# Kernel tuning notes

Measured on AMD Instinct MI355X. Metric: run time of the kernel, lower is better.

Reference implementation:

```python
import jax, jax.numpy as jnp
import numpy as np

B, N, C, G, K = 4, 6000, 91, 32, 100
IMG = 800.0
SCORE_TH = 0.05
NMS_TH = 0.5
MATCH_TH = 0.5
MIN_SIZE = 0.01
BBOX_CLIP = float(np.log(1000.0 / 16.0))
WX, WY, WW, WH = 10.0, 10.0, 5.0, 5.0


def _make_boxes(key, shape_prefix):
    k1, k2 = jax.random.split(key)
    xy = jax.random.uniform(k1, shape_prefix + (2,), minval=0.0, maxval=IMG - 130.0)
    wh = jax.random.uniform(k2, shape_prefix + (2,), minval=8.0, maxval=128.0)
    return jnp.concatenate([xy, xy + wh], axis=-1)


def setup_inputs() -> dict:
    key = jax.random.key(0)
    k1, k2, k3, k4, k5 = jax.random.split(key, 5)
    return {
        "class_logits": 2.0 * jax.random.normal(k1, (B * N, C), dtype=jnp.float32),
        "box_regression": jax.random.normal(k2, (B * N, C * 4), dtype=jnp.float32),
        "proposals": _make_boxes(k3, (B, N)),
        "gt_boxes": _make_boxes(k4, (B, G)),
        "gt_labels": jax.random.randint(k5, (B, G), 1, C),
    }


def _box_iou(a, b):
    # a [G,4], b [N,4] -> [G,N]
    area_a = (a[:, 2] - a[:, 0]) * (a[:, 3] - a[:, 1])
    area_b = (b[:, 2] - b[:, 0]) * (b[:, 3] - b[:, 1])
    lt = jnp.maximum(a[:, None, :2], b[None, :, :2])
    rb = jnp.minimum(a[:, None, 2:], b[None, :, 2:])
    wh = jnp.clip(rb - lt, 0.0)
    inter = wh[..., 0] * wh[..., 1]
    return inter / (area_a[:, None] + area_b[None, :] - inter)


def _decode(rel, props):
    # torchvision BoxCoder.decode; rel [N,C,4], props [N,4]
    w = props[:, 2] - props[:, 0]
    h = props[:, 3] - props[:, 1]
    cx = props[:, 0] + 0.5 * w
    cy = props[:, 1] + 0.5 * h
    dx = rel[..., 0] / WX
    dy = rel[..., 1] / WY
    dw = jnp.minimum(rel[..., 2] / WW, BBOX_CLIP)
    dh = jnp.minimum(rel[..., 3] / WH, BBOX_CLIP)
    pcx = dx * w[:, None] + cx[:, None]
    pcy = dy * h[:, None] + cy[:, None]
    pw = jnp.exp(dw) * w[:, None]
    ph = jnp.exp(dh) * h[:, None]
    return jnp.stack([pcx - 0.5 * pw, pcy - 0.5 * ph, pcx + 0.5 * pw, pcy + 0.5 * ph], axis=-1)


def _image(logits, reg, props, gtb, gtl):
    # --- assign_targets_to_proposals (Matcher, low=high=0.5, no low-quality matches) ---
    iou = _box_iou(gtb, props)                      # [G, N]
    best = iou.max(axis=0)
    mi = jnp.argmax(iou, axis=0)
    matched = jnp.where(best >= MATCH_TH, mi, -1)   # -1 == BELOW_LOW_THRESHOLD
    assigned = jnp.where(matched >= 0, gtl[jnp.clip(matched, 0)], 0)

    # --- postprocess_detections ---
    scores = jax.nn.softmax(logits, axis=-1)[:, 1:].reshape(-1)                       # [N*(C-1)]
    boxes = jnp.clip(_decode(reg.reshape(N, C, 4), props)[:, 1:], 0.0, IMG)
    boxes = boxes.reshape(-1, 4)                                                      # [N*(C-1),4]
    labels = jnp.tile(jnp.arange(1, C), N)                                            # [N*(C-1)]
    ws = boxes[:, 2] - boxes[:, 0]
    hs = boxes[:, 3] - boxes[:, 1]
    valid = (scores > SCORE_TH) & (ws >= MIN_SIZE) & (hs >= MIN_SIZE)
    s0 = jnp.where(valid, scores, -jnp.inf)
    # batched_nms trick: offset boxes by label so cross-class IoU is 0
    off = boxes + (labels.astype(boxes.dtype) * (IMG + 1.0))[:, None]
    off_area = (off[:, 2] - off[:, 0]) * (off[:, 3] - off[:, 1])

    def step(s, _):
        i = jnp.argmax(s)
        sc = s[i]
        b = off[i]
        lt = jnp.maximum(off[:, :2], b[:2])
        rb = jnp.minimum(off[:, 2:], b[2:])
        wh = jnp.clip(rb - lt, 0.0)
        inter = wh[:, 0] * wh[:, 1]
        iou_all = inter / (off_area + (b[2] - b[0]) * (b[3] - b[1]) - inter)
        s = jnp.where(iou_all > NMS_TH, -jnp.inf, s)  # suppress (includes self)
        ok = jnp.isfinite(sc)
        ob = jnp.where(ok, boxes[i], 0.0)
        osc = jnp.where(ok, sc, 0.0)
        ol = jnp.where(ok, labels[i], -1)
        return s, (ob, osc, ol)

    _, (kb, ksc, kl) = jax.lax.scan(step, s0, None, length=K)
    return kb, ksc, kl, assigned, matched


def reference(class_logits, box_regression, proposals, gt_boxes, gt_labels):
    logits = class_logits.reshape(B, N, C)
    reg = box_regression.reshape(B, N, C * 4)
    kb, ksc, kl, assigned, matched = jax.vmap(_image)(logits, reg, proposals, gt_boxes, gt_labels)
    dets = jnp.concatenate([kb, ksc[..., None]], axis=-1)  # [B, K, 5]
    return dets, kl, assigned, matched
```

## Files before the change

kernel.cpp:

```cpp
#include <hip/hip_runtime.h>
#include <math.h>

#define NB 4
#define NN 6000
#define NC 91
#define NG 32
#define NK 100
#define NCLS (NC - 1)
#define NBUC (NB * NCLS)
#define SLOTS_MAX 2048
#define CUR_STRIDE 32
#define PMAX 512
#define MATW 256
#define MPB 4096
#define RS_BLOCKS 6000

#define SCORE_TH 0.05f
#define NMS_TH 0.5f
#define MATCH_TH 0.5f
#define MIN_SIZE 0.01f
#define BBOX_CLIP 4.135166556742356f
#define C_SUP 0.5000000298023223876953125

#define CFENCE() asm volatile("" ::: "memory")

__device__ __forceinline__ bool decode_one(
    const float* __restrict__ reg, const float* __restrict__ props,
    float l, float m, float s0, int row, int c, float out[5])
{
    float score = __fdiv_rn(expf(__fsub_rn(l, m)), s0);

    const float4 p = *reinterpret_cast<const float4*>(props + (size_t)row * 4);
    float w  = __fsub_rn(p.z, p.x);
    float h  = __fsub_rn(p.w, p.y);
    float cx = __fadd_rn(p.x, __fmul_rn(0.5f, w));
    float cy = __fadd_rn(p.y, __fmul_rn(0.5f, h));

    const float4 r4 = *reinterpret_cast<const float4*>(
        reg + (size_t)row * (NC * 4) + (size_t)c * 4);
    float dx = __fdiv_rn(r4.x, 10.0f);
    float dy = __fdiv_rn(r4.y, 10.0f);
    float dw = fminf(__fdiv_rn(r4.z, 5.0f), BBOX_CLIP);
    float dh = fminf(__fdiv_rn(r4.w, 5.0f), BBOX_CLIP);

    float pcx = __fadd_rn(__fmul_rn(dx, w), cx);
    float pcy = __fadd_rn(__fmul_rn(dy, h), cy);
    float pw  = __fmul_rn(expf(dw), w);
    float ph  = __fmul_rn(expf(dh), h);

    float x1 = __fsub_rn(pcx, __fmul_rn(0.5f, pw));
    float y1 = __fsub_rn(pcy, __fmul_rn(0.5f, ph));
    float x2 = __fadd_rn(pcx, __fmul_rn(0.5f, pw));
    float y2 = __fadd_rn(pcy, __fmul_rn(0.5f, ph));
    x1 = fminf(fmaxf(x1, 0.0f), 800.0f);
    y1 = fminf(fmaxf(y1, 0.0f), 800.0f);
    x2 = fminf(fmaxf(x2, 0.0f), 800.0f);
    y2 = fminf(fmaxf(y2, 0.0f), 800.0f);

    out[0] = score; out[1] = x1; out[2] = y1; out[3] = x2; out[4] = y2;
    float ws_ = __fsub_rn(x2, x1);
    float hs_ = __fsub_rn(y2, y1);
    return (score > SCORE_TH) && (ws_ >= MIN_SIZE) && (hs_ >= MIN_SIZE);
}

__global__ __launch_bounds__(256) void fused_kernel(
    const float* __restrict__ logits, const float* __restrict__ reg,
    const float* __restrict__ props, const float* __restrict__ gtb,
    const int* __restrict__ gtl,
    float* __restrict__ out_assigned, float* __restrict__ out_matched,
    int* __restrict__ cursors, float* __restrict__ ent, int slots)
{
    int bid = blockIdx.x;
    if (bid < RS_BLOCKS) {
        int wid = threadIdx.x >> 6, lane = threadIdx.x & 63;
        int row = bid * 4 + wid;
        const float* rp = logits + (size_t)row * NC;
        float l0 = rp[lane];
        float l1 = (lane < NC - 64) ? rp[64 + lane] : -INFINITY;
        float m = fmaxf(fmaxf(-INFINITY, l0), l1);
        for (int o = 32; o; o >>= 1) m = fmaxf(m, __shfl_down(m, o));
        m = __shfl(m, 0);
        float s = __fadd_rn(__fadd_rn(0.0f, expf(__fsub_rn(l0, m))),
                            expf(__fsub_rn(l1, m)));
        for (int o = 32; o; o >>= 1) s = __fadd_rn(s, __shfl_down(s, o));
        float s0 = __shfl(s, 0);
        float thr = __fadd_rn(m, logf(__fmul_rn(0.04f, s0)));

        int b = row / NN;
        int nprop = row - b * NN;

        if (lane >= 1 && l0 > thr) {
            float o[5];
            if (decode_one(reg, props, l0, m, s0, row, lane, o)) {
                int c = lane;
                int g = b * NCLS + (c - 1);
                int pos = atomicAdd(&cursors[g * CUR_STRIDE], 1);
                if (pos < slots) {
                    float* e = ent + ((size_t)g * slots + pos) * 8;
                    *reinterpret_cast<float4*>(e) =
                        make_float4(o[1], o[2], o[3], o[4]);
                    *reinterpret_cast<float2*>(e + 4) =
                        make_float2(o[0], (float)(nprop * NCLS + (c - 1)));
                }
            }
        }
        if (lane < NC - 64 && l1 > thr) {
            float o[5];
            int c = lane + 64;
            if (decode_one(reg, props, l1, m, s0, row, c, o)) {
                int g = b * NCLS + (c - 1);
                int pos = atomicAdd(&cursors[g * CUR_STRIDE], 1);
                if (pos < slots) {
                    float* e = ent + ((size_t)g * slots + pos) * 8;
                    *reinterpret_cast<float4*>(e) =
                        make_float4(o[1], o[2], o[3], o[4]);
                    *reinterpret_cast<float2*>(e + 4) =
                        make_float2(o[0], (float)(nprop * NCLS + (c - 1)));
                }
            }
        }
    } else {
        int t = (bid - RS_BLOCKS) * 256 + threadIdx.x;
        if (t >= NB * NN) return;
        int b = t / NN;
        const float4 p = *reinterpret_cast<const float4*>(props + (size_t)t * 4);
        float parea = __fmul_rn(__fsub_rn(p.z, p.x), __fsub_rn(p.w, p.y));
        float best = -1.0f; int bi = -1;
        for (int g = 0; g < NG; ++g) {
            const float4 q = *reinterpret_cast<const float4*>(gtb + ((size_t)b * NG + g) * 4);
            float garea = __fmul_rn(__fsub_rn(q.z, q.x), __fsub_rn(q.w, q.y));
            float ltx = fmaxf(q.x, p.x), lty = fmaxf(q.y, p.y);
            float rbx = fminf(q.z, p.z), rby = fminf(q.w, p.w);
            float wx = fmaxf(__fsub_rn(rbx, ltx), 0.0f);
            float wy = fmaxf(__fsub_rn(rby, lty), 0.0f);
            float inter = __fmul_rn(wx, wy);
            float iou = __fdiv_rn(inter, __fsub_rn(__fadd_rn(garea, parea), inter));
            if (iou > best) { best = iou; bi = g; }
        }
        int matched = (best >= MATCH_TH) ? bi : -1;
        int assigned = (matched >= 0) ? gtl[b * NG + matched] : 0;
        out_matched[t]  = (float)matched;
        out_assigned[t] = (float)assigned;
    }
}

__device__ void nms_glb(int g, int n, float* __restrict__ E, float tb, float cls,
                        float* __restrict__ selbuf, int* __restrict__ selcnt)
{
    int lane = threadIdx.x & 63;
    int kout = 0;
    for (int k = 0; k < NK; ++k) {
        float bv = -INFINITY, boi = INFINITY; int bi = -1;
        for (int i = lane; i < n; i += 64) {
            float v = E[(size_t)i * 8 + 4], oi = E[(size_t)i * 8 + 5];
            if (v > bv || (v == bv && oi < boi)) { bv = v; boi = oi; bi = i; }
        }
        int wl = lane;
        for (int o = 1; o < 64; o <<= 1) {
            float v2 = __shfl_xor(bv, o); float o2 = __shfl_xor(boi, o);
            int l2 = __shfl_xor(wl, o);
            bool bt = (v2 > bv) || (v2 == bv && o2 < boi);
            bv = bt ? v2 : bv; boi = bt ? o2 : boi; wl = bt ? l2 : wl;
        }
        if (bv == -INFINITY) break;
        int wi = __shfl(bi, wl);
        float sx1 = E[(size_t)wi * 8 + 0], sy1 = E[(size_t)wi * 8 + 1];
        float sx2 = E[(size_t)wi * 8 + 2], sy2 = E[(size_t)wi * 8 + 3];
        if (lane == wl) {
            float* so = selbuf + ((size_t)g * NK + k) * 8;
            so[0] = bv; so[1] = sx1; so[2] = sy1; so[3] = sx2; so[4] = sy2;
            so[5] = cls; so[6] = boi; so[7] = 0.0f;
        }
        float bx1 = __fadd_rn(sx1, tb), by1 = __fadd_rn(sy1, tb);
        float bx2 = __fadd_rn(sx2, tb), by2 = __fadd_rn(sy2, tb);
        float sar = __fmul_rn(__fsub_rn(bx2, bx1), __fsub_rn(by2, by1));
        for (int i = lane; i < n; i += 64) {
            float v = E[(size_t)i * 8 + 4];
            if (v == -INFINITY) continue;
            float ox1 = __fadd_rn(E[(size_t)i * 8 + 0], tb);
            float oy1 = __fadd_rn(E[(size_t)i * 8 + 1], tb);
            float ox2 = __fadd_rn(E[(size_t)i * 8 + 2], tb);
            float oy2 = __fadd_rn(E[(size_t)i * 8 + 3], tb);
            float oar = __fmul_rn(__fsub_rn(ox2, ox1), __fsub_rn(oy2, oy1));
            float ltx = fmaxf(ox1, bx1), lty = fmaxf(oy1, by1);
            float rbx = fminf(ox2, bx2), rby = fminf(oy2, by2);
            float wx = fmaxf(__fsub_rn(rbx, ltx), 0.0f);
            float wy = fmaxf(__fsub_rn(rby, lty), 0.0f);
            float inter = __fmul_rn(wx, wy);
            float den = __fsub_rn(__fadd_rn(oar, sar), inter);
            if ((double)inter > C_SUP * (double)den) E[(size_t)i * 8 + 4] = -INFINITY;
        }
        kout = k + 1;
    }
    if (lane == 0) selcnt[g] = kout;
}

template <int CAP>
__device__ __forceinline__ float selN(const float a[CAP], int j) {
    float r = a[0];
#pragma unroll
    for (int i = 1; i < CAP; ++i) r = (j == i) ? a[i] : r;
    return r;
}
__device__ __forceinline__ float rdlane(float v, int l) {
    return __uint_as_float(
        (unsigned)__builtin_amdgcn_readlane((int)__float_as_uint(v), l));
}
__device__ __forceinline__ unsigned long long rdlane64(unsigned long long v, int l) {
    unsigned lo = (unsigned)__builtin_amdgcn_readlane((int)(unsigned)v, l);
    unsigned hi = (unsigned)__builtin_amdgcn_readlane((int)(unsigned)(v >> 32), l);
    return ((unsigned long long)hi << 32) | lo;
}

template <int CAP>
__device__ __forceinline__ int sweep_reg(
    int lane, int n, float tb,
    const float* sx1, const float* sy1, const float* sx2, const float* sy2,
    int* acc)
{
    float ox1[CAP], oy1[CAP], ox2[CAP], oy2[CAP], oar[CAP];
    unsigned alive = 0;
#pragma unroll
    for (int j = 0; j < CAP; ++j) {
        int sidx = lane * CAP + j;
        if (sidx < n) {
            float a  = __fadd_rn(sx1[sidx], tb);
            float b_ = __fadd_rn(sy1[sidx], tb);
            float c_ = __fadd_rn(sx2[sidx], tb);
            float d_ = __fadd_rn(sy2[sidx], tb);
            ox1[j] = a; oy1[j] = b_; ox2[j] = c_; oy2[j] = d_;
            oar[j] = __fmul_rn(__fsub_rn(c_, a), __fsub_rn(d_, b_));
            alive |= 1u << j;
        } else {
            ox1[j] = 0.f; oy1[j] = 0.f; ox2[j] = 0.f; oy2[j] = 0.f; oar[j] = 0.f;
        }
    }
    int kout = 0;
    while (kout < NK) {
        unsigned long long bal = __ballot(alive != 0u);
        if (!bal) break;
        int fl = (int)__ffsll(bal) - 1;
        unsigned am = (unsigned)__builtin_amdgcn_readlane((int)alive, fl);
        int js = __ffs(am) - 1;
        float bx1 = rdlane(selN<CAP>(ox1, js), fl);
        float by1 = rdlane(selN<CAP>(oy1, js), fl);
        float bx2 = rdlane(selN<CAP>(ox2, js), fl);
        float by2 = rdlane(selN<CAP>(oy2, js), fl);
        float bar = rdlane(selN<CAP>(oar, js), fl);
        if (lane == 0) acc[kout] = fl * CAP + js;
        kout++;
        unsigned kill = 0;
#pragma unroll
        for (int j = 0; j < CAP; ++j) {
            float ltx = fmaxf(ox1[j], bx1), lty = fmaxf(oy1[j], by1);
            float rbx = fminf(ox2[j], bx2), rby = fminf(oy2[j], by2);
            float wx = fmaxf(__fsub_rn(rbx, ltx), 0.0f);
            float wy = fmaxf(__fsub_rn(rby, lty), 0.0f);
            float inter = __fmul_rn(wx, wy);
            float den = __fsub_rn(__fadd_rn(oar[j], bar), inter);
            if ((double)inter > C_SUP * (double)den) kill |= 1u << j;
        }
        alive &= ~kill;
    }
    return kout;
}

__global__ __launch_bounds__(512) void bucket_nms_kernel(
    const int* __restrict__ cursors, int slots,
    float* __restrict__ entries,
    float* __restrict__ selbuf, int* __restrict__ selcnt)
{
    int g = blockIdx.x;
    int n = cursors[g * CUR_STRIDE]; if (n > slots) n = slots;
    int tid = threadIdx.x;
    if (n == 0) { if (tid == 0) selcnt[g] = 0; return; }
    float* E = entries + (size_t)g * slots * 8;
    float cls = (float)(g % NCLS + 1);
    float tb = __fmul_rn(cls, 801.0f);

    if (n > PMAX) {
        if (tid < 64) nms_glb(g, n, E, tb, cls, selbuf, selcnt);
        return;
    }

    __shared__ unsigned skhi[PMAX], sklo[PMAX];
    __shared__ int sperm[PMAX];
    __shared__ float sx1[PMAX], sy1[PMAX], sx2[PMAX], sy2[PMAX];
    __shared__ unsigned long long dmask[MATW * 4];
    __shared__ int acc[NK];
    __shared__ int s_kout, s_fb;

    int P = 64; while (P < n) P <<= 1;

    for (int i = tid; i < P; i += 512) {
        if (i < n) {
            const float2 kv = *reinterpret_cast<const float2*>(E + (size_t)i * 8 + 4);
            skhi[i] = __float_as_uint(kv.x);
            sklo[i] = ~((unsigned)kv.y);
        } else { skhi[i] = 0u; sklo[i] = 0u; }
        sperm[i] = i;
    }
    __syncthreads();
    for (int k = 2; k <= P; k <<= 1) {
        for (int j = k >> 1; j > 0; j >>= 1) {
            bool cross = (j >= 128);
            if (cross) __syncthreads();
            for (int t = tid; t < (P >> 1); t += 512) {
                int i = ((t & ~(j - 1)) << 1) | (t & (j - 1));
                int l = i | j;
                unsigned ah = skhi[i], al = sklo[i], ch = skhi[l], cl_ = sklo[l];
                bool alt = (ah < ch) || (ah == ch && al < cl_);
                bool agt = (ah > ch) || (ah == ch && al > cl_);
                bool sw = ((i & k) == 0) ? alt : agt;
                if (sw) {
                    skhi[i] = ch; sklo[i] = cl_; skhi[l] = ah; sklo[l] = al;
                    int tp = sperm[i]; sperm[i] = sperm[l]; sperm[l] = tp;
                }
            }
            if (cross) __syncthreads();
            else CFENCE();
        }
    }
    __syncthreads();
    for (int i = tid; i < n; i += 512) {
        const float4 v = *reinterpret_cast<const float4*>(E + (size_t)sperm[i] * 8);
        sx1[i] = v.x; sy1[i] = v.y; sx2[i] = v.z; sy2[i] = v.w;
    }
    __syncthreads();

    int W = (n < MATW) ? n : MATW;
    int nchunk = (W + 63) >> 6;
    int wv = tid >> 6, lane = tid & 63;

    float jx1[4], jy1[4], jx2[4], jy2[4], jar[4];
#pragma unroll
    for (int c = 0; c < 4; ++c) {
        int j = c * 64 + lane;
        if (j < W) {
            float a  = __fadd_rn(sx1[j], tb);
            float b_ = __fadd_rn(sy1[j], tb);
            float c_ = __fadd_rn(sx2[j], tb);
            float d_ = __fadd_rn(sy2[j], tb);
            jx1[c] = a; jy1[c] = b_; jx2[c] = c_; jy2[c] = d_;
            jar[c] = __fmul_rn(__fsub_rn(c_, a), __fsub_rn(d_, b_));
        } else {
            jx1[c] = 0.f; jy1[c] = 0.f; jx2[c] = 0.f; jy2[c] = 0.f; jar[c] = 0.f;
        }
    }
    {
        int i0 = wv;
        float nx1 = 0.f, ny1 = 0.f, nx2 = 0.f, ny2 = 0.f;
        if (i0 < W) { nx1 = sx1[i0]; ny1 = sy1[i0]; nx2 = sx2[i0]; ny2 = sy2[i0]; }
        for (int i = i0; i < W; i += 8) {
            float rx1 = nx1, ry1 = ny1, rx2 = nx2, ry2 = ny2;
            int ni = i + 8;
            if (ni < W) { nx1 = sx1[ni]; ny1 = sy1[ni]; nx2 = sx2[ni]; ny2 = sy2[ni]; }
            float bx1 = __fadd_rn(rx1, tb), by1 = __fadd_rn(ry1, tb);
            float bx2 = __fadd_rn(rx2, tb), by2 = __fadd_rn(ry2, tb);
            float bar = __fmul_rn(__fsub_rn(bx2, bx1), __fsub_rn(by2, by1));
            int ic = i >> 6;
#pragma unroll
            for (int c = 0; c < 4; ++c) {
                if (c >= ic && c < nchunk) {
                    bool jv = (c * 64 + lane) < W;
                    float ltx = fmaxf(jx1[c], bx1), lty = fmaxf(jy1[c], by1);
                    float rbx = fminf(jx2[c], bx2), rby = fminf(jy2[c], by2);
                    float wx = fmaxf(__fsub_rn(rbx, ltx), 0.0f);
                    float wy = fmaxf(__fsub_rn(rby, lty), 0.0f);
                    float inter = __fmul_rn(wx, wy);
                    float den = __fsub_rn(__fadd_rn(jar[c], bar), inter);
                    bool sup = jv && ((double)inter > C_SUP * (double)den);
                    unsigned long long w64 = __ballot(sup);
                    if (lane == 0) dmask[i * 4 + c] = w64;
                }
            }
        }
    }
    __syncthreads();

    if (tid < 64) {
        unsigned long long a0 = 0, a1 = 0, a2 = 0, a3 = 0;
        {
            int rem = W;
            a0 = (rem >= 64) ? ~0ull : ((rem > 0) ? ((1ull << rem) - 1) : 0); rem -= 64;
            a1 = (rem >= 64) ? ~0ull : ((rem > 0) ? ((1ull << rem) - 1) : 0); rem -= 64;
            a2 = (rem >= 64) ? ~0ull : ((rem > 0) ? ((1ull << rem) - 1) : 0); rem -= 64;
            a3 = (rem >= 64) ? ~0ull : ((rem > 0) ? ((1ull << rem) - 1) : 0);
        }
        int kout = 0;
        while (kout < NK) {
            int cand;
            if      (a0) cand = (int)__ffsll(a0) - 1;
            else if (a1) cand = 64  + (int)__ffsll(a1) - 1;
            else if (a2) cand = 128 + (int)__ffsll(a2) - 1;
            else if (a3) cand = 192 + (int)__ffsll(a3) - 1;
            else break;
            if (lane == 0) acc[kout] = cand;
            kout++;
            unsigned long long mrow = (lane < 4) ? dmask[cand * 4 + lane] : 0ull;
            a0 &= ~rdlane64(mrow, 0);
            a1 &= ~rdlane64(mrow, 1);
            a2 &= ~rdlane64(mrow, 2);
            a3 &= ~rdlane64(mrow, 3);
        }
        if (lane == 0) {
            s_kout = kout;
            s_fb = (kout < NK && n > W) ? 1 : 0;
        }
    }
    __syncthreads();

    if (s_fb) {
        if (tid < 64) {
            int kout = sweep_reg<8>(lane, n, tb, sx1, sy1, sx2, sy2, acc);
            if (lane == 0) s_kout = kout;
        }
        __syncthreads();
    }

    int kc = s_kout;
    if (tid == 0) selcnt[g] = kc;
    for (int k = tid; k < kc; k += 512) {
        int cand = acc[k];
        float* so = selbuf + ((size_t)g * NK + k) * 8;
        so[0] = __uint_as_float(skhi[cand]);
        so[1] = sx1[cand]; so[2] = sy1[cand];
        so[3] = sx2[cand]; so[4] = sy2[cand];
        so[5] = cls; so[6] = (float)(~sklo[cand]); so[7] = 0.0f;
    }
}

__global__ __launch_bounds__(512) void merge_kernel(
    const float* __restrict__ selbuf, const int* __restrict__ selcnt,
    float* __restrict__ out_dets, float* __restrict__ out_kl)
{
    int b = blockIdx.x, tid = threadIdx.x;
    __shared__ int scnt[NCLS], soff[NCLS + 1];
    __shared__ unsigned akhi[512], aklo[512];
    __shared__ unsigned bkhi[MPB], bklo[MPB], bpay[MPB];
    __shared__ int s_T, s_cntA;
    __shared__ unsigned s_LBhi, s_LBlo;

    if (tid < NCLS) scnt[tid] = selcnt[b * NCLS + tid];
    if (tid == 0) s_T = 0;
    __syncthreads();
    if (tid == 0) {
        int a = 0, ca = 0;
        for (int c = 0; c < NCLS; ++c) {
            soff[c] = a; a += scnt[c];
            ca += (scnt[c] < 4 ? scnt[c] : 4);
        }
        soff[NCLS] = a; s_cntA = ca;
    }
    __syncthreads();
    int tot = soff[NCLS];

    if (tot == 0) {
        for (int z = tid; z < NK * 5; z += 512) out_dets[(size_t)b * NK * 5 + z] = 0.0f;
        for (int z = tid; z < NK; z += 512)     out_kl[(size_t)b * NK + z] = -1.0f;
        return;
    }

    {
        unsigned kh = 0u, kl = 0u;
        if (tid < NCLS * 4) {
            int c = tid >> 2, i = tid & 3;
            if (i < scnt[c]) {
                const float* e = selbuf + ((size_t)(b * NCLS + c) * NK + i) * 8;
                kh = __float_as_uint(e[0]); kl = ~((unsigned)e[6]);
            }
        }
        akhi[tid] = kh; aklo[tid] = kl;
    }
    __syncthreads();
    for (int k = 2; k <= 512; k <<= 1) {
        for (int j = k >> 1; j > 0; j >>= 1) {
            bool cross = (j >= 128);
            if (cross) __syncthreads();
            if (tid < 256) {
                int t = tid;
                int i = ((t & ~(j - 1)) << 1) | (t & (j - 1));
                int l = i | j;
                unsigned ah = akhi[i], al = aklo[i], ch = akhi[l], cl_ = aklo[l];
                bool alt = (ah < ch) || (ah == ch && al < cl_);
                bool agt = (ah > ch) || (ah == ch && al > cl_);
                bool sw = ((i & k) == 0) ? alt : agt;
                if (sw) {
                    akhi[i] = ch; aklo[i] = cl_; akhi[l] = ah; aklo[l] = al;
                }
            }
            if (cross) __syncthreads();
            else CFENCE();
        }
    }
    __syncthreads();
    if (tid == 0) {
        if (s_cntA >= NK) { s_LBhi = akhi[NK - 1]; s_LBlo = aklo[NK - 1]; }
        else              { s_LBhi = 0u;           s_LBlo = 0u; }
    }
    __syncthreads();
    unsigned LBhi = s_LBhi, LBlo = s_LBlo;

    for (int flat = tid; flat < tot; flat += 512) {
        int lo = 0, hi = NCLS - 1;
        while (lo < hi) { int mid = (lo + hi + 1) >> 1;
                          if (soff[mid] <= flat) lo = mid; else hi = mid - 1; }
        int c = lo, i = flat - soff[c];
        const float* e = selbuf + ((size_t)(b * NCLS + c) * NK + i) * 8;
        unsigned kh = __float_as_uint(e[0]), kl = ~((unsigned)e[6]);
        bool ge = (kh > LBhi) || (kh == LBhi && kl >= LBlo);
        if (ge) {
            int pos = atomicAdd(&s_T, 1);
            if (pos < MPB) { bkhi[pos] = kh; bklo[pos] = kl;
                             bpay[pos] = (unsigned)((c << 7) | i); }
        }
    }
    __syncthreads();
    int T = s_T;

    if (T > MPB) {
        if (tid >= 64) return;
        int lane = tid;
        int g0 = b * NCLS + lane;
        int g1 = (lane < NCLS - 64) ? g0 + 64 : -1;
        int c0 = scnt[lane];
        int c1 = (g1 >= 0) ? scnt[lane + 64] : 0;
        int p0 = 0, p1 = 0;
        unsigned long long k0c = 0, k1c = 0;
        if (p0 < c0) { const float* h = selbuf + ((size_t)g0 * NK) * 8;
            k0c = ((unsigned long long)__float_as_uint(h[0]) << 32) | (unsigned long long)(~(unsigned)h[6]); }
        if (g1 >= 0 && p1 < c1) { const float* h = selbuf + ((size_t)g1 * NK) * 8;
            k1c = ((unsigned long long)__float_as_uint(h[0]) << 32) | (unsigned long long)(~(unsigned)h[6]); }
        for (int k = 0; k < NK; ++k) {
            bool t1 = (k1c > k0c);
            unsigned long long bk = t1 ? k1c : k0c;
            int bslot = t1 ? (lane + 64) : lane;
            for (int o = 1; o < 64; o <<= 1) {
                unsigned long long k2 = __shfl_xor(bk, o);
                int b2 = __shfl_xor(bslot, o);
                if (k2 > bk) { bk = k2; bslot = b2; }
            }
            if (bk == 0ull) {
                for (int z = k * 5 + lane; z < NK * 5; z += 64)
                    out_dets[(size_t)b * NK * 5 + z] = 0.0f;
                for (int z = k + lane; z < NK; z += 64)
                    out_kl[(size_t)b * NK + z] = -1.0f;
                return;
            }
            int owner = bslot & 63;
            if (lane == owner) {
                bool isA = (bslot < 64);
                int gg = isA ? g0 : g1;
                int pp = isA ? p0 : p1;
                const float* e = selbuf + ((size_t)gg * NK + pp) * 8;
                size_t o = ((size_t)b * NK + k) * 5;
                out_dets[o + 0] = e[1]; out_dets[o + 1] = e[2];
                out_dets[o + 2] = e[3]; out_dets[o + 3] = e[4];
                out_dets[o + 4] = e[0];
                out_kl[(size_t)b * NK + k] = e[5];
                if (isA) {
                    p0++; k0c = 0;
                    if (p0 < c0) { const float* h = selbuf + ((size_t)g0 * NK + p0) * 8;
                        k0c = ((unsigned long long)__float_as_uint(h[0]) << 32) | (unsigned long long)(~(unsigned)h[6]); }
                } else {
                    p1++; k1c = 0;
                    if (p1 < c1) { const float* h = selbuf + ((size_t)g1 * NK + p1) * 8;
                        k1c = ((unsigned long long)__float_as_uint(h[0]) << 32) | (unsigned long long)(~(unsigned)h[6]); }
                }
            }
        }
        return;
    }

    int P = 128; while (P < T) P <<= 1;
    for (int i = T + tid; i < P; i += 512) { bkhi[i] = 0u; bklo[i] = 0u; bpay[i] = 0u; }
    __syncthreads();
    for (int k = 2; k <= P; k <<= 1) {
        for (int j = k >> 1; j > 0; j >>= 1) {
            bool cross = (j >= 128);
            if (cross) __syncthreads();
            for (int t = tid; t < (P >> 1); t += 512) {
                int i = ((t & ~(j - 1)) << 1) | (t & (j - 1));
                int l = i | j;
                unsigned ah = bkhi[i], al = bklo[i], ch = bkhi[l], cl_ = bklo[l];
                bool alt = (ah < ch) || (ah == ch && al < cl_);
                bool agt = (ah > ch) || (ah == ch && al > cl_);
                bool sw = ((i & k) == 0) ? alt : agt;
                if (sw) {
                    bkhi[i] = ch; bklo[i] = cl_; bkhi[l] = ah; bklo[l] = al;
                    unsigned tp = bpay[i]; bpay[i] = bpay[l]; bpay[l] = tp;
                }
            }
            if (cross) __syncthreads();
            else CFENCE();
        }
    }
    __syncthreads();
    int kc = (T < NK) ? T : NK;
    for (int k = tid; k < NK; k += 512) {
        size_t o = ((size_t)b * NK + k) * 5;
        if (k < kc) {
            unsigned pay = bpay[k];
            int c = (int)(pay >> 7), p = (int)(pay & 127);
            const float* e = selbuf + ((size_t)(b * NCLS + c) * NK + p) * 8;
            out_dets[o + 0] = e[1]; out_dets[o + 1] = e[2];
            out_dets[o + 2] = e[3]; out_dets[o + 3] = e[4];
            out_dets[o + 4] = e[0];
            out_kl[(size_t)b * NK + k] = e[5];
        } else {
            out_dets[o + 0] = 0.0f; out_dets[o + 1] = 0.0f;
            out_dets[o + 2] = 0.0f; out_dets[o + 3] = 0.0f;
            out_dets[o + 4] = 0.0f;
            out_kl[(size_t)b * NK + k] = -1.0f;
        }
    }
}

extern "C" void kernel_launch(void* const* d_in, const int* in_sizes, int n_in,
                              void* d_out, int out_size, void* d_ws, size_t ws_size,
                              hipStream_t stream) {
    const float* logits = (const float*)d_in[0];
    const float* reg    = (const float*)d_in[1];
    const float* props  = (const float*)d_in[2];
    const float* gtb    = (const float*)d_in[3];
    const int*   gtl    = (const int*)d_in[4];

    float* out          = (float*)d_out;
    float* out_dets     = out;
    float* out_kl       = out + NB * NK * 5;
    float* out_assigned = out_kl + NB * NK;
    float* out_matched  = out_assigned + NB * NN;

    char* ws = (char*)d_ws;
    int*   cursors = (int*)(ws + 0);
    int*   selcnt  = (int*)(ws + 49152);
    float* selbuf  = (float*)(ws + 53248);
    size_t off_ent = 1205248;

    long avail = (long)ws_size - (long)off_ent;
    long per_slot = 32L * NBUC;
    long slotsl = (avail > 0) ? avail / per_slot : 0;
    int slots = (int)((slotsl > SLOTS_MAX) ? SLOTS_MAX : (slotsl < 0 ? 0 : slotsl));

    float* entries = (float*)(ws + off_ent);

    hipMemsetAsync(cursors, 0, NBUC * CUR_STRIDE * sizeof(int), stream);
    const int MATCH_BLOCKS = (NB * NN + 255) / 256;
    fused_kernel<<<RS_BLOCKS + MATCH_BLOCKS, 256, 0, stream>>>(
        logits, reg, props, gtb, gtl, out_assigned, out_matched,
        cursors, entries, slots);
    bucket_nms_kernel<<<NBUC, 512, 0, stream>>>(
        cursors, slots, entries, selbuf, selcnt);
    merge_kernel<<<NB, 512, 0, stream>>>(selbuf, selcnt, out_dets, out_kl);
}
```

Baseline: 118.8 us.

## Replace atomic bucket cursors with dense per-proposal flag array and compaction

Candidate detections are now written to a fixed slot indexed by proposal within each class bucket and marked in a byte flag array, instead of being appended through global atomic cursors. The NMS kernel scans the 6000 flags per bucket and compacts them into shared memory with shared atomics before sorting. This removes contended global atomics and the slot-capacity limit. In exchange it adds a memset of 360×6000 bytes, a full flag scan per bucket, and a much larger entries buffer, and the compaction order is now nondeterministic, which the sort must absorb.

```diff
diff --git a/kernel.cpp b/kernel.cpp
--- a/kernel.cpp
+++ b/kernel.cpp
@@ -8,8 +8,6 @@
 #define NK 100
 #define NCLS (NC - 1)
 #define NBUC (NB * NCLS)
-#define SLOTS_MAX 2048
-#define CUR_STRIDE 32
 #define PMAX 512
 #define MATW 256
 #define MPB 4096
@@ -68,7 +66,7 @@
     const float* __restrict__ props, const float* __restrict__ gtb,
     const int* __restrict__ gtl,
     float* __restrict__ out_assigned, float* __restrict__ out_matched,
-    int* __restrict__ cursors, float* __restrict__ ent, int slots)
+    unsigned char* __restrict__ flags, float* __restrict__ ent)
 {
     int bid = blockIdx.x;
     if (bid < RS_BLOCKS) {
@@ -92,16 +90,14 @@
         if (lane >= 1 && l0 > thr) {
             float o[5];
             if (decode_one(reg, props, l0, m, s0, row, lane, o)) {
-                int c = lane;
-                int g = b * NCLS + (c - 1);
-                int pos = atomicAdd(&cursors[g * CUR_STRIDE], 1);
-                if (pos < slots) {
-                    float* e = ent + ((size_t)g * slots + pos) * 8;
-                    *reinterpret_cast<float4*>(e) =
-                        make_float4(o[1], o[2], o[3], o[4]);
-                    *reinterpret_cast<float2*>(e + 4) =
-                        make_float2(o[0], (float)(nprop * NCLS + (c - 1)));
-                }
+                int g = b * NCLS + (lane - 1);
+                size_t sl = (size_t)g * NN + nprop;
+                float* e = ent + sl * 8;
+                *reinterpret_cast<float4*>(e) =
+                    make_float4(o[1], o[2], o[3], o[4]);
+                *reinterpret_cast<float2*>(e + 4) =
+                    make_float2(o[0], (float)(nprop * NCLS + (lane - 1)));
+                flags[sl] = 1;
             }
         }
         if (lane < NC - 64 && l1 > thr) {
@@ -109,14 +105,13 @@
             int c = lane + 64;
             if (decode_one(reg, props, l1, m, s0, row, c, o)) {
                 int g = b * NCLS + (c - 1);
-                int pos = atomicAdd(&cursors[g * CUR_STRIDE], 1);
-                if (pos < slots) {
-                    float* e = ent + ((size_t)g * slots + pos) * 8;
-                    *reinterpret_cast<float4*>(e) =
-                        make_float4(o[1], o[2], o[3], o[4]);
-                    *reinterpret_cast<float2*>(e + 4) =
-                        make_float2(o[0], (float)(nprop * NCLS + (c - 1)));
-                }
+                size_t sl = (size_t)g * NN + nprop;
+                float* e = ent + sl * 8;
+                *reinterpret_cast<float4*>(e) =
+                    make_float4(o[1], o[2], o[3], o[4]);
+                *reinterpret_cast<float2*>(e + 4) =
+                    make_float2(o[0], (float)(nprop * NCLS + (c - 1)));
+                flags[sl] = 1;
             }
         }
     } else {
@@ -144,14 +139,16 @@
     }
 }
 
-__device__ void nms_glb(int g, int n, float* __restrict__ E, float tb, float cls,
-                        float* __restrict__ selbuf, int* __restrict__ selcnt)
+__device__ void nms_glb_sparse(int g, const unsigned char* __restrict__ F,
+                               float* __restrict__ E, float tb, float cls,
+                               float* __restrict__ selbuf, int* __restrict__ selcnt)
 {
     int lane = threadIdx.x & 63;
     int kout = 0;
     for (int k = 0; k < NK; ++k) {
         float bv = -INFINITY, boi = INFINITY; int bi = -1;
-        for (int i = lane; i < n; i += 64) {
+        for (int i = lane; i < NN; i += 64) {
+            if (!F[i]) continue;
             float v = E[(size_t)i * 8 + 4], oi = E[(size_t)i * 8 + 5];
             if (v > bv || (v == bv && oi < boi)) { bv = v; boi = oi; bi = i; }
         }
@@ -174,7 +171,8 @@
         float bx1 = __fadd_rn(sx1, tb), by1 = __fadd_rn(sy1, tb);
         float bx2 = __fadd_rn(sx2, tb), by2 = __fadd_rn(sy2, tb);
         float sar = __fmul_rn(__fsub_rn(bx2, bx1), __fsub_rn(by2, by1));
-        for (int i = lane; i < n; i += 64) {
+        for (int i = lane; i < NN; i += 64) {
+            if (!F[i]) continue;
             float v = E[(size_t)i * 8 + 4];
             if (v == -INFINITY) continue;
             float ox1 = __fadd_rn(E[(size_t)i * 8 + 0], tb);
@@ -266,23 +264,19 @@
 }
 
 __global__ __launch_bounds__(512) void bucket_nms_kernel(
-    const int* __restrict__ cursors, int slots,
+    const unsigned char* __restrict__ flags,
     float* __restrict__ entries,
     float* __restrict__ selbuf, int* __restrict__ selcnt)
 {
     int g = blockIdx.x;
-    int n = cursors[g * CUR_STRIDE]; if (n > slots) n = slots;
     int tid = threadIdx.x;
-    if (n == 0) { if (tid == 0) selcnt[g] = 0; return; }
-    float* E = entries + (size_t)g * slots * 8;
+    float* E = entries + (size_t)g * NN * 8;
+    const unsigned char* F = flags + (size_t)g * NN;
     float cls = (float)(g % NCLS + 1);
     float tb = __fmul_rn(cls, 801.0f);
 
-    if (n > PMAX) {
-        if (tid < 64) nms_glb(g, n, E, tb, cls, selbuf, selcnt);
-        return;
-    }
-
+    __shared__ int sidx[PMAX];
+    __shared__ int s_n;
     __shared__ unsigned skhi[PMAX], sklo[PMAX];
     __shared__ int sperm[PMAX];
     __shared__ float sx1[PMAX], sy1[PMAX], sx2[PMAX], sy2[PMAX];
@@ -290,11 +284,29 @@
     __shared__ int acc[NK];
     __shared__ int s_kout, s_fb;
 
+    if (tid == 0) s_n = 0;
+    __syncthreads();
+    for (int i = tid; i < NN; i += 512) {
+        if (F[i]) {
+            int p = atomicAdd(&s_n, 1);
+            if (p < PMAX) sidx[p] = i;
+        }
+    }
+    __syncthreads();
+    int ntot = s_n;
+    if (ntot == 0) { if (tid == 0) selcnt[g] = 0; return; }
+    if (ntot > PMAX) {
+        if (tid < 64) nms_glb_sparse(g, F, E, tb, cls, selbuf, selcnt);
+        return;
+    }
+    int n = ntot;
+
     int P = 64; while (P < n) P <<= 1;
 
     for (int i = tid; i < P; i += 512) {
         if (i < n) {
-            const float2 kv = *reinterpret_cast<const float2*>(E + (size_t)i * 8 + 4);
+            const float2 kv = *reinterpret_cast<const float2*>(
+                E + (size_t)sidx[i] * 8 + 4);
             skhi[i] = __float_as_uint(kv.x);
             sklo[i] = ~((unsigned)kv.y);
         } else { skhi[i] = 0u; sklo[i] = 0u; }
@@ -323,7 +335,8 @@
     }
     __syncthreads();
     for (int i = tid; i < n; i += 512) {
-        const float4 v = *reinterpret_cast<const float4*>(E + (size_t)sperm[i] * 8);
+        const float4 v = *reinterpret_cast<const float4*>(
+            E + (size_t)sidx[sperm[i]] * 8);
         sx1[i] = v.x; sy1[i] = v.y; sx2[i] = v.z; sy2[i] = v.w;
     }
     __syncthreads();
@@ -632,24 +645,17 @@
     float* out_matched  = out_assigned + NB * NN;
 
     char* ws = (char*)d_ws;
-    int*   cursors = (int*)(ws + 0);
-    int*   selcnt  = (int*)(ws + 49152);
-    float* selbuf  = (float*)(ws + 53248);
-    size_t off_ent = 1205248;
-
-    long avail = (long)ws_size - (long)off_ent;
-    long per_slot = 32L * NBUC;
-    long slotsl = (avail > 0) ? avail / per_slot : 0;
-    int slots = (int)((slotsl > SLOTS_MAX) ? SLOTS_MAX : (slotsl < 0 ? 0 : slotsl));
-
-    float* entries = (float*)(ws + off_ent);
-
-    hipMemsetAsync(cursors, 0, NBUC * CUR_STRIDE * sizeof(int), stream);
+    int*   selcnt  = (int*)(ws + 0);
+    float* selbuf  = (float*)(ws + 65536);
+    unsigned char* flags = (unsigned char*)(ws + 2097152);
+    float* entries = (float*)(ws + 8388608);
+
+    hipMemsetAsync(flags, 0, (size_t)NBUC * NN, stream);
     const int MATCH_BLOCKS = (NB * NN + 255) / 256;
     fused_kernel<<<RS_BLOCKS + MATCH_BLOCKS, 256, 0, stream>>>(
         logits, reg, props, gtb, gtl, out_assigned, out_matched,
-        cursors, entries, slots);
+        flags, entries);
     bucket_nms_kernel<<<NBUC, 512, 0, stream>>>(
-        cursors, slots, entries, selbuf, selcnt);
+        flags, entries, selbuf, selcnt);
     merge_kernel<<<NB, 512, 0, stream>>>(selbuf, selcnt, out_dets, out_kl);
 }
```

Measured after the change: 119.3 us. No clear change (+0.4%).
